# Kernel tuning notes

Hardware: AMD Instinct MI355X
Metric: run time of the kernel (lower is better)

Reference implementation:

```python
import jax, jax.numpy as jnp
import numpy as np

DIM = 1024
NUM_HEADS = 16
HEAD_DIM = DIM // NUM_HEADS


def setup_inputs() -> dict:
    key = jax.random.key(0)
    k1, k2, k3, k4, k5 = jax.random.split(key, 5)
    scale = 0.02
    return {
        "x": jax.random.normal(k1, (4, 2048, DIM), dtype=jnp.float32),
        "w_qkv": jax.random.normal(k2, (DIM, 3 * DIM), dtype=jnp.float32) * scale,
        "b_qkv": jax.random.normal(k3, (3 * DIM,), dtype=jnp.float32) * scale,
        "w_proj": jax.random.normal(k4, (DIM, DIM), dtype=jnp.float32) * scale,
        "b_proj": jax.random.normal(k5, (DIM,), dtype=jnp.float32) * scale,
    }


def reference(x, w_qkv, b_qkv, w_proj, b_proj):
    B, N, C = x.shape
    H, D = NUM_HEADS, HEAD_DIM
    qkv = x @ w_qkv + b_qkv                      # [B, N, 3C]
    qkv = qkv.reshape(B, N, 3, H, D)
    q = qkv[:, :, 0].transpose(0, 2, 1, 3)       # [B, H, N, D]
    k = qkv[:, :, 1].transpose(0, 2, 1, 3)
    v = qkv[:, :, 2].transpose(0, 2, 1, 3)
    attn = jnp.einsum("bhnd,bhmd->bhnm", q, k) / (D ** 0.5)  # [B, H, N, N]
    attn = jax.nn.softmax(attn, axis=-1)
    out = jnp.einsum("bhnm,bhmd->bhnd", attn, v)  # [B, H, N, D]
    out = out.transpose(0, 2, 1, 3).reshape(B, N, C)
    return out @ w_proj + b_proj
```

## Files before the change

kernel.cpp:

```cpp
#include <hip/hip_runtime.h>
#include <stdint.h>

typedef __bf16 bf16_t;
typedef __bf16 bf16x8 __attribute__((ext_vector_type(8)));
typedef __bf16 bf16x4 __attribute__((ext_vector_type(4)));
typedef float  f32x4  __attribute__((ext_vector_type(4)));

__device__ __forceinline__ void g2l16(const void* g, void* l) {
    __builtin_amdgcn_global_load_lds(
        (const __attribute__((address_space(1))) unsigned int*)g,
        (__attribute__((address_space(3))) unsigned int*)l, 16, 0, 0);
}

__global__ __launch_bounds__(256) void prep_kernel(
    const float* __restrict__ x, const float* __restrict__ w_qkv,
    const float* __restrict__ w_proj,
    bf16_t* __restrict__ x_bf, bf16_t* __restrict__ wqkvT, bf16_t* __restrict__ wprojT)
{
    __shared__ float t[32][33];
    const int bx = blockIdx.x;
    if (bx < 8192) {
        const int idx = (bx * 256 + threadIdx.x) * 4;
        const float4 v = *(const float4*)(x + idx);
        bf16x4 o;
        o[0] = (bf16_t)v.x; o[1] = (bf16_t)v.y; o[2] = (bf16_t)v.z; o[3] = (bf16_t)v.w;
        *(bf16x4*)(x_bf + idx) = o;
        return;
    }
    const float* in;
    bf16_t* outp;
    int c0, r0, C;
    if (bx < 11264) {
        const int b = bx - 8192;
        in = w_qkv; outp = wqkvT; C = 3072;
        c0 = (b % 96) * 32; r0 = (b / 96) * 32;
    } else {
        const int b = bx - 11264;
        in = w_proj; outp = wprojT; C = 1024;
        c0 = (b & 31) * 32; r0 = (b >> 5) * 32;
    }
    const int xx = threadIdx.x & 31, y = threadIdx.x >> 5;
    #pragma unroll
    for (int i = 0; i < 32; i += 8)
        t[y + i][xx] = in[(size_t)(r0 + y + i) * C + c0 + xx];
    __syncthreads();
    #pragma unroll
    for (int i = 0; i < 32; i += 8)
        outp[(size_t)(c0 + y + i) * 1024 + r0 + xx] = (bf16_t)t[xx][y + i];
}

__device__ __forceinline__ void gemm128(
    const bf16_t* __restrict__ A, const bf16_t* __restrict__ Bt, const int K,
    bf16_t* sA, bf16_t* sB, const int m0, const int n0, f32x4 acc[4][4])
{
    const int tid  = threadIdx.x;
    const int lane = tid & 63;
    const int w    = tid >> 6;
    const int wm   = (w >> 1) * 64;
    const int wn   = (w & 1) * 64;
    const int col0 = lane & 15;
    const int quad = lane >> 4;

    #pragma unroll
    for (int mt = 0; mt < 4; ++mt)
        #pragma unroll
        for (int nt = 0; nt < 4; ++nt)
            acc[mt][nt] = (f32x4){0.f, 0.f, 0.f, 0.f};

    const int srow = tid >> 3;
    const int jsw  = ((tid & 7) ^ (srow & 7)) << 3;
    const bf16_t* Ab = A  + (size_t)(m0 + srow) * K + jsw;
    const bf16_t* Bb = Bt + (size_t)(n0 + srow) * K + jsw;

    for (int kb = 0; kb < K; kb += 64) {
        #pragma unroll
        for (int it = 0; it < 4; ++it) {
            g2l16(Ab + (size_t)(it * 32) * K + kb, sA + (size_t)(it * 256 + tid) * 8);
            g2l16(Bb + (size_t)(it * 32) * K + kb, sB + (size_t)(it * 256 + tid) * 8);
        }
        __syncthreads();
        #pragma unroll
        for (int ks = 0; ks < 2; ++ks) {
            const int jg = ks * 4 + quad;
            bf16x8 af[4], bv[4];
            #pragma unroll
            for (int mt = 0; mt < 4; ++mt) {
                const int ra = wm + mt * 16 + col0;
                af[mt] = *(const bf16x8*)(sA + ra * 64 + ((jg ^ (ra & 7)) << 3));
            }
            #pragma unroll
            for (int nt = 0; nt < 4; ++nt) {
                const int rb = wn + nt * 16 + col0;
                bv[nt] = *(const bf16x8*)(sB + rb * 64 + ((jg ^ (rb & 7)) << 3));
            }
            #pragma unroll
            for (int mt = 0; mt < 4; ++mt)
                #pragma unroll
                for (int nt = 0; nt < 4; ++nt)
                    acc[mt][nt] = __builtin_amdgcn_mfma_f32_16x16x32_bf16(
                        af[mt], bv[nt], acc[mt][nt], 0, 0, 0);
        }
        __syncthreads();
    }
}

#define QSCALE 0.18033688f
__global__ __launch_bounds__(256) void qkv_gemm_kernel(
    const bf16_t* __restrict__ x, const bf16_t* __restrict__ wT,
    const float* __restrict__ bias,
    bf16_t* __restrict__ q, bf16_t* __restrict__ k, bf16_t* __restrict__ vT)
{
    __shared__ bf16_t sA[128 * 64];
    __shared__ bf16_t sB[128 * 64];
    const int m0 = blockIdx.y * 128;
    const int n0 = blockIdx.x * 128;
    f32x4 acc[4][4];
    gemm128(x, wT, 1024, sA, sB, m0, n0, acc);

    const int tid = threadIdx.x, lane = tid & 63, w = tid >> 6;
    const int wm = (w >> 1) * 64, wn = (w & 1) * 64;
    const int col0 = lane & 15, quad = lane >> 4;
    const int sel = n0 >> 10;

    #pragma unroll
    for (int mt = 0; mt < 4; ++mt) {
        const int m_base = m0 + wm + mt * 16 + quad * 4;
        const int b = m_base >> 11;
        const int t = m_base & 2047;
        #pragma unroll
        for (int nt = 0; nt < 4; ++nt) {
            const int n = n0 + wn + nt * 16 + col0;
            const float bvv = bias[n];
            const int h = (n >> 6) & 15, d = n & 63;
            const size_t bh = (size_t)b * 16 + h;
            if (sel == 0) {
                #pragma unroll
                for (int r = 0; r < 4; ++r)
                    q[(bh * 2048 + t + r) * 64 + d] = (bf16_t)((acc[mt][nt][r] + bvv) * QSCALE);
            } else if (sel == 1) {
                #pragma unroll
                for (int r = 0; r < 4; ++r)
                    k[(bh * 2048 + t + r) * 64 + d] = (bf16_t)(acc[mt][nt][r] + bvv);
            } else {
                #pragma unroll
                for (int r = 0; r < 4; ++r)
                    vT[(bh * 64 + d) * 2048 + t + r] = (bf16_t)(acc[mt][nt][r] + bvv);
            }
        }
    }
}

__global__ __launch_bounds__(256) void proj_gemm_kernel(
    const bf16_t* __restrict__ a, const bf16_t* __restrict__ wT,
    const float* __restrict__ bias, float* __restrict__ out)
{
    __shared__ bf16_t sA[128 * 64];
    __shared__ bf16_t sB[128 * 64];
    const int m0 = blockIdx.y * 128;
    const int n0 = blockIdx.x * 128;
    f32x4 acc[4][4];
    gemm128(a, wT, 1024, sA, sB, m0, n0, acc);

    const int tid = threadIdx.x, lane = tid & 63, w = tid >> 6;
    const int wm = (w >> 1) * 64, wn = (w & 1) * 64;
    const int col0 = lane & 15, quad = lane >> 4;
    #pragma unroll
    for (int mt = 0; mt < 4; ++mt) {
        const int m_base = m0 + wm + mt * 16 + quad * 4;
        #pragma unroll
        for (int nt = 0; nt < 4; ++nt) {
            const int n = n0 + wn + nt * 16 + col0;
            const float bvv = bias[n];
            #pragma unroll
            for (int r = 0; r < 4; ++r)
                out[(size_t)(m_base + r) * 1024 + n] = acc[mt][nt][r] + bvv;
        }
    }
}

__global__ __launch_bounds__(256, 4) void attn_kernel(
    const bf16_t* __restrict__ q, const bf16_t* __restrict__ k,
    const bf16_t* __restrict__ vT, bf16_t* __restrict__ out)
{
    __shared__ __align__(16) char smem[16384 + 16384];
    bf16_t* sK = (bf16_t*)smem;
    bf16_t* sV = (bf16_t*)(smem + 16384);

    const int x   = blockIdx.x;
    const int loc = x >> 3;
    const int qb  = loc & 15;
    const int bh  = (x & 7) + ((loc >> 4) << 3);

    const int tid = threadIdx.x, lane = tid & 63, w = tid >> 6;
    const int col0 = lane & 15, quad = lane >> 4;

    const bf16_t* qbase = q  + ((size_t)bh * 2048 + qb * 128) * 64;
    const bf16_t* kbase = k  + (size_t)bh * 2048 * 64;
    const bf16_t* vbase = vT + (size_t)bh * 64 * 2048;

    const int srow8  = tid >> 3;
    const int jsw8   = ((tid & 7) ^ (srow8 & 7)) << 3;
    const int srow16 = tid >> 4;
    const int jsw16  = ((tid & 15) ^ (srow16 & 15)) << 3;

    bf16x8 qf[2][2];
    #pragma unroll
    for (int mt = 0; mt < 2; ++mt)
        #pragma unroll
        for (int ks = 0; ks < 2; ++ks)
            qf[mt][ks] = *(const bf16x8*)(qbase
                + (size_t)(w * 32 + mt * 16 + col0) * 64 + ks * 32 + quad * 8);

    bf16x8 kr[4], vr[4];
    #pragma unroll
    for (int it = 0; it < 4; ++it)
        kr[it] = *(const bf16x8*)(kbase + (size_t)(it * 32 + srow8) * 64 + jsw8);
    #pragma unroll
    for (int it = 0; it < 4; ++it)
        vr[it] = *(const bf16x8*)(vbase + (size_t)(it * 16 + srow16) * 2048 + jsw16);

    f32x4 oacc[2][4];
    float row_l[2];
    #pragma unroll
    for (int mt = 0; mt < 2; ++mt) {
        #pragma unroll
        for (int nt = 0; nt < 4; ++nt) oacc[mt][nt] = (f32x4){0.f, 0.f, 0.f, 0.f};
        row_l[mt] = 0.f;
    }

    for (int kv = 0; kv < 16; ++kv) {
        __syncthreads();
        #pragma unroll
        for (int it = 0; it < 4; ++it)
            *(bf16x8*)(sK + (size_t)(it * 256 + tid) * 8) = kr[it];
        #pragma unroll
        for (int it = 0; it < 4; ++it)
            *(bf16x8*)(sV + (size_t)(it * 256 + tid) * 8) = vr[it];
        __syncthreads();

        if (kv < 15) {
            const bf16_t* kg = kbase + (size_t)(kv + 1) * 128 * 64;
            #pragma unroll
            for (int it = 0; it < 4; ++it)
                kr[it] = *(const bf16x8*)(kg + (size_t)(it * 32 + srow8) * 64 + jsw8);
            #pragma unroll
            for (int it = 0; it < 4; ++it)
                vr[it] = *(const bf16x8*)(vbase + (size_t)(it * 16 + srow16) * 2048
                                          + (kv + 1) * 128 + jsw16);
        }

        #pragma unroll
        for (int hf = 0; hf < 2; ++hf) {
            f32x4 s[4][2];
            #pragma unroll
            for (int nt = 0; nt < 4; ++nt)
                #pragma unroll
                for (int mt = 0; mt < 2; ++mt) s[nt][mt] = (f32x4){0.f, 0.f, 0.f, 0.f};
            #pragma unroll
            for (int ks = 0; ks < 2; ++ks) {
                const int jg = ks * 4 + quad;
                bf16x8 kf[4];
                #pragma unroll
                for (int nt = 0; nt < 4; ++nt) {
                    const int rk = hf * 64 + nt * 16 + col0;
                    kf[nt] = *(const bf16x8*)(sK + rk * 64 + ((jg ^ (rk & 7)) << 3));
                }
                #pragma unroll
                for (int nt = 0; nt < 4; ++nt)
                    #pragma unroll
                    for (int mt = 0; mt < 2; ++mt)
                        s[nt][mt] = __builtin_amdgcn_mfma_f32_16x16x32_bf16(
                            kf[nt], qf[mt][ks], s[nt][mt], 0, 0, 0);
            }

            unsigned pw[2][2][4];
            #pragma unroll
            for (int mt = 0; mt < 2; ++mt) {
                #pragma unroll
                for (int kp = 0; kp < 2; ++kp) {
                    float p0[4], p1[4];
                    float rs = 0.f;
                    #pragma unroll
                    for (int r = 0; r < 4; ++r) {
                        p0[r] = __builtin_amdgcn_exp2f(s[2 * kp][mt][r]);
                        p1[r] = __builtin_amdgcn_exp2f(s[2 * kp + 1][mt][r]);
                        rs += p0[r] + p1[r];
                    }
                    row_l[mt] += rs;
                    unsigned XA, XB, YA, YB;
                    asm("v_cvt_pk_bf16_f32 %0, %1, %2" : "=v"(XA) : "v"(p0[0]), "v"(p0[1]));
                    asm("v_cvt_pk_bf16_f32 %0, %1, %2" : "=v"(XB) : "v"(p0[2]), "v"(p0[3]));
                    asm("v_cvt_pk_bf16_f32 %0, %1, %2" : "=v"(YA) : "v"(p1[0]), "v"(p1[1]));
                    asm("v_cvt_pk_bf16_f32 %0, %1, %2" : "=v"(YB) : "v"(p1[2]), "v"(p1[3]));
                    asm("v_permlane32_swap_b32 %0, %1" : "+v"(XA), "+v"(YA));
                    asm("v_permlane16_swap_b32 %0, %1" : "+v"(XA), "+v"(YA));
                    asm("v_permlane32_swap_b32 %0, %1" : "+v"(XB), "+v"(YB));
                    asm("v_permlane16_swap_b32 %0, %1" : "+v"(XB), "+v"(YB));
                    pw[mt][kp][0] = XA; pw[mt][kp][1] = XB;
                    pw[mt][kp][2] = YA; pw[mt][kp][3] = YB;
                }
            }

            #pragma unroll
            for (int kp = 0; kp < 2; ++kp) {
                const int jg2 = (hf * 2 + kp) * 4 + quad;
                bf16x8 vf[4];
                #pragma unroll
                for (int nt = 0; nt < 4; ++nt) {
                    const int dv = nt * 16 + col0;
                    vf[nt] = *(const bf16x8*)(sV + dv * 128 + ((jg2 ^ (dv & 15)) << 3));
                }
                #pragma unroll
                for (int mt = 0; mt < 2; ++mt) {
                    union { unsigned wds[4]; bf16x8 v; } u;
                    u.wds[0] = pw[mt][kp][0]; u.wds[1] = pw[mt][kp][1];
                    u.wds[2] = pw[mt][kp][2]; u.wds[3] = pw[mt][kp][3];
                    #pragma unroll
                    for (int nt = 0; nt < 4; ++nt)
                        oacc[mt][nt] = __builtin_amdgcn_mfma_f32_16x16x32_bf16(
                            u.v, vf[nt], oacc[mt][nt], 0, 0, 0);
                }
            }
        }
    }

    float lt[2];
    #pragma unroll
    for (int mt = 0; mt < 2; ++mt) {
        float l = row_l[mt];
        l += __shfl_xor(l, 16);
        l += __shfl_xor(l, 32);
        lt[mt] = l;
    }
    const int b = bh >> 4, h = bh & 15;
    #pragma unroll
    for (int mt = 0; mt < 2; ++mt) {
        #pragma unroll
        for (int r = 0; r < 4; ++r) {
            const float inv = 1.0f / __shfl(lt[mt], quad * 4 + r);
            const int t = qb * 128 + w * 32 + mt * 16 + quad * 4 + r;
            const size_t rowbase = ((size_t)b * 2048 + t) * 1024 + h * 64;
            #pragma unroll
            for (int nt = 0; nt < 4; ++nt)
                out[rowbase + nt * 16 + col0] = (bf16_t)(oacc[mt][nt][r] * inv);
        }
    }
}

extern "C" void kernel_launch(void* const* d_in, const int* in_sizes, int n_in,
                              void* d_out, int out_size, void* d_ws, size_t ws_size,
                              hipStream_t stream) {
    const float* x      = (const float*)d_in[0];
    const float* w_qkv  = (const float*)d_in[1];
    const float* b_qkv  = (const float*)d_in[2];
    const float* w_proj = (const float*)d_in[3];
    const float* b_proj = (const float*)d_in[4];
    float* out = (float*)d_out;

    char* p = (char*)d_ws;
    bf16_t* x_bf   = (bf16_t*)p; p += (size_t)8192 * 1024 * 2;
    bf16_t* wqkvT  = (bf16_t*)p; p += (size_t)3072 * 1024 * 2;
    bf16_t* wprojT = (bf16_t*)p; p += (size_t)1024 * 1024 * 2;
    bf16_t* qb     = (bf16_t*)p; p += (size_t)8192 * 1024 * 2;
    bf16_t* kb     = (bf16_t*)p; p += (size_t)8192 * 1024 * 2;
    bf16_t* vTb    = (bf16_t*)p; p += (size_t)8192 * 1024 * 2;
    bf16_t* attb   = (bf16_t*)p; p += (size_t)8192 * 1024 * 2;

    prep_kernel<<<12288, 256, 0, stream>>>(x, w_qkv, w_proj, x_bf, wqkvT, wprojT);
    qkv_gemm_kernel<<<dim3(24, 64), 256, 0, stream>>>(x_bf, wqkvT, b_qkv, qb, kb, vTb);
    attn_kernel<<<1024, 256, 0, stream>>>(qb, kb, vTb, attb);
    proj_gemm_kernel<<<dim3(8, 64), 256, 0, stream>>>(attb, wprojT, b_proj, out);
}
```

Before: 317.6 us.

## Load K/V tiles directly to LDS and interleave softmax with PV MFMAs

Replaces the register-staged K/V prefetch, where the next tile is held in registers and then written to LDS, with direct global-to-LDS loads issued at the start of each KV iteration, followed by a barrier before compute and another at the end. It also merges the softmax/pack loop into the PV loop, so packed probabilities feed the MFMAs at once instead of being kept in a pw array. This cuts VGPR pressure and the LDS store instructions. The cost is that global load latency is no longer overlapped with the previous tile's compute, since there is only a single buffer.

Result: faster. 271.2 us (-14.6%).

```diff
diff --git a/kernel.cpp b/kernel.cpp
--- a/kernel.cpp
+++ b/kernel.cpp
@@ -211,14 +211,6 @@
             qf[mt][ks] = *(const bf16x8*)(qbase
                 + (size_t)(w * 32 + mt * 16 + col0) * 64 + ks * 32 + quad * 8);
 
-    bf16x8 kr[4], vr[4];
-    #pragma unroll
-    for (int it = 0; it < 4; ++it)
-        kr[it] = *(const bf16x8*)(kbase + (size_t)(it * 32 + srow8) * 64 + jsw8);
-    #pragma unroll
-    for (int it = 0; it < 4; ++it)
-        vr[it] = *(const bf16x8*)(vbase + (size_t)(it * 16 + srow16) * 2048 + jsw16);
-
     f32x4 oacc[2][4];
     float row_l[2];
     #pragma unroll
@@ -229,25 +221,16 @@
     }
 
     for (int kv = 0; kv < 16; ++kv) {
+        const bf16_t* kg = kbase + (size_t)kv * 128 * 64;
+        #pragma unroll
+        for (int it = 0; it < 4; ++it)
+            g2l16(kg + (size_t)(it * 32 + srow8) * 64 + jsw8,
+                  sK + (size_t)(it * 256 + tid) * 8);
+        #pragma unroll
+        for (int it = 0; it < 4; ++it)
+            g2l16(vbase + (size_t)(it * 16 + srow16) * 2048 + kv * 128 + jsw16,
+                  sV + (size_t)(it * 256 + tid) * 8);
         __syncthreads();
-        #pragma unroll
-        for (int it = 0; it < 4; ++it)
-            *(bf16x8*)(sK + (size_t)(it * 256 + tid) * 8) = kr[it];
-        #pragma unroll
-        for (int it = 0; it < 4; ++it)
-            *(bf16x8*)(sV + (size_t)(it * 256 + tid) * 8) = vr[it];
-        __syncthreads();
-
-        if (kv < 15) {
-            const bf16_t* kg = kbase + (size_t)(kv + 1) * 128 * 64;
-            #pragma unroll
-            for (int it = 0; it < 4; ++it)
-                kr[it] = *(const bf16x8*)(kg + (size_t)(it * 32 + srow8) * 64 + jsw8);
-            #pragma unroll
-            for (int it = 0; it < 4; ++it)
-                vr[it] = *(const bf16x8*)(vbase + (size_t)(it * 16 + srow16) * 2048
-                                          + (kv + 1) * 128 + jsw16);
-        }
 
         #pragma unroll
         for (int hf = 0; hf < 2; ++hf) {
@@ -273,11 +256,17 @@
                             kf[nt], qf[mt][ks], s[nt][mt], 0, 0, 0);
             }
 
-            unsigned pw[2][2][4];
-            #pragma unroll
-            for (int mt = 0; mt < 2; ++mt) {
-                #pragma unroll
-                for (int kp = 0; kp < 2; ++kp) {
+            #pragma unroll
+            for (int kp = 0; kp < 2; ++kp) {
+                const int jg2 = (hf * 2 + kp) * 4 + quad;
+                bf16x8 vf[4];
+                #pragma unroll
+                for (int nt = 0; nt < 4; ++nt) {
+                    const int dv = nt * 16 + col0;
+                    vf[nt] = *(const bf16x8*)(sV + dv * 128 + ((jg2 ^ (dv & 15)) << 3));
+                }
+                #pragma unroll
+                for (int mt = 0; mt < 2; ++mt) {
                     float p0[4], p1[4];
                     float rs = 0.f;
                     #pragma unroll
@@ -296,25 +285,8 @@
                     asm("v_permlane16_swap_b32 %0, %1" : "+v"(XA), "+v"(YA));
                     asm("v_permlane32_swap_b32 %0, %1" : "+v"(XB), "+v"(YB));
                     asm("v_permlane16_swap_b32 %0, %1" : "+v"(XB), "+v"(YB));
-                    pw[mt][kp][0] = XA; pw[mt][kp][1] = XB;
-                    pw[mt][kp][2] = YA; pw[mt][kp][3] = YB;
-                }
-            }
-
-            #pragma unroll
-            for (int kp = 0; kp < 2; ++kp) {
-                const int jg2 = (hf * 2 + kp) * 4 + quad;
-                bf16x8 vf[4];
-                #pragma unroll
-                for (int nt = 0; nt < 4; ++nt) {
-                    const int dv = nt * 16 + col0;
-                    vf[nt] = *(const bf16x8*)(sV + dv * 128 + ((jg2 ^ (dv & 15)) << 3));
-                }
-                #pragma unroll
-                for (int mt = 0; mt < 2; ++mt) {
                     union { unsigned wds[4]; bf16x8 v; } u;
-                    u.wds[0] = pw[mt][kp][0]; u.wds[1] = pw[mt][kp][1];
-                    u.wds[2] = pw[mt][kp][2]; u.wds[3] = pw[mt][kp][3];
+                    u.wds[0] = XA; u.wds[1] = XB; u.wds[2] = YA; u.wds[3] = YB;
                     #pragma unroll
                     for (int nt = 0; nt < 4; ++nt)
                         oacc[mt][nt] = __builtin_amdgcn_mfma_f32_16x16x32_bf16(
@@ -322,6 +294,7 @@
                 }
             }
         }
+        __syncthreads();
     }
 
     float lt[2];
```
